# Optimization experiments

Measured on AMD Instinct MI355X. Metric: run time of the kernel, lower is better.

The kernel has to match this reference:

```python
import math
import jax, jax.numpy as jnp
import numpy as np

B, QC, KC, RES, SRC = 4, 512, 256, 64, 128
T = RES * RES


def setup_inputs():
    key = jax.random.key(0)
    ks = jax.random.split(key, 8)
    return {
        "key_feat": jax.random.normal(ks[0], (B, KC, SRC, SRC), jnp.float32),
        "query": jax.random.normal(ks[1], (B, QC, RES, RES), jnp.float32),
        "Weight_Mat": jax.random.uniform(ks[2], (B, T, T), dtype=jnp.float32),
        "key_proj_w": jax.random.normal(ks[3], (QC, KC), jnp.float32) * 0.02,
        "norm_w": jnp.ones((QC,), jnp.float32),
        "norm_b": jnp.zeros((QC,), jnp.float32),
        "qkv_w": jax.random.normal(ks[4], (3 * QC, 2 * QC), jnp.float32) * 0.02,
        "qkv_b": jax.random.normal(ks[5], (3 * QC,), jnp.float32) * 0.02,
        "proj_w": jax.random.normal(ks[6], (QC, QC), jnp.float32) * 0.02,
        "proj_b": jnp.zeros((QC,), jnp.float32),
    }


def group_norm(x, w, b, groups=32, eps=1e-5):
    # x: (b, C, L) -- GroupNorm over channel groups and spatial dim
    bs, C, L = x.shape
    xg = x.reshape(bs, groups, C // groups, L)
    mu = xg.mean(axis=(2, 3), keepdims=True)
    var = xg.var(axis=(2, 3), keepdims=True)
    xn = ((xg - mu) * jax.lax.rsqrt(var + eps)).reshape(bs, C, L)
    return xn * w[None, :, None] + b[None, :, None]


def reference(key_feat, query, Weight_Mat, key_proj_w, norm_w, norm_b, qkv_w, qkv_b, proj_w, proj_b):
    b, qc, H, W = query.shape
    f = key_feat.shape[2] // H  # exact integer downsample factor (2)
    # F.interpolate bilinear (align_corners=False) at exact 1/f rate == f x f average pooling
    kds = key_feat.reshape(b, key_feat.shape[1], H, f, W, f).mean(axis=(3, 5))
    # Weight_Mat interpolate has scale==1 in source (no-op), elided.
    k = jnp.einsum('oc,bchw->bohw', key_proj_w, kds).reshape(b, qc, H * W)
    q = query.reshape(b, qc, H * W)
    q = group_norm(q, norm_w, norm_b)
    k = group_norm(k, norm_w, norm_b)
    # qkv: 1x1 conv1d on concat(q, k) -> (b, 3*qc, T)
    qkv = jnp.einsum('oc,bct->bot', qkv_w, jnp.concatenate([q, k], axis=1)) + qkv_b[None, :, None]
    qq, kk, vv = jnp.split(qkv, 3, axis=1)  # each (b, qc, T); num_heads=1 so ch=qc
    scale = qc ** -0.25  # 1/sqrt(sqrt(ch))
    logits = Weight_Mat * jnp.einsum('bct,bcs->bts', qq * scale, kk * scale)
    attn = jax.nn.softmax(logits, axis=-1)
    a = jnp.einsum('bts,bcs->bct', attn, vv)
    h = jnp.einsum('oc,bct->bot', proj_w, a) + proj_b[None, :, None]
    # residual uses the NORMALIZED query, as in the source
    return (q + h).reshape(b, qc, H, W)
```

## Files before the change

kernel.cpp:

```cpp
#include <hip/hip_runtime.h>
#include <hip/hip_bf16.h>
#include <stdint.h>

#define NB 4
#define CQ 512
#define CK 256
#define TT 4096
#define SCALE_QK 0.21022410381342863f

using bf16x8 = __attribute__((ext_vector_type(8))) short;
using f32x4  = __attribute__((ext_vector_type(4))) float;
using u32x4  = __attribute__((ext_vector_type(4))) unsigned int;
typedef unsigned short u16;

__device__ __forceinline__ u16 f2bf(float f) {
    union { float f; unsigned u; } v; v.f = f;
    return (u16)((v.u + 0x7fffu + ((v.u >> 16) & 1u)) >> 16);
}
__device__ __forceinline__ float bf2f(u16 h) {
    union { float f; unsigned u; } v; v.u = ((unsigned)h) << 16;
    return v.f;
}
__device__ __forceinline__ bf16x8 pack8(f32x4 a, f32x4 b) {
    bf16x8 r;
    r[0] = (short)f2bf(a[0]); r[1] = (short)f2bf(a[1]);
    r[2] = (short)f2bf(a[2]); r[3] = (short)f2bf(a[3]);
    r[4] = (short)f2bf(b[0]); r[5] = (short)f2bf(b[1]);
    r[6] = (short)f2bf(b[2]); r[7] = (short)f2bf(b[3]);
    return r;
}
__device__ __forceinline__ void gload_lds16(const void* g, void* l) {
    __builtin_amdgcn_global_load_lds(
        (const __attribute__((address_space(1))) unsigned int*)g,
        (__attribute__((address_space(3))) unsigned int*)l, 16, 0, 0);
}

__global__ __launch_bounds__(256) void wconv_kernel(const float* __restrict__ src,
        u16* __restrict__ dst, int n, int scale_until) {
    int i = (blockIdx.x * 256 + threadIdx.x) * 8;
    if (i >= n) return;
    f32x4 a = *(const f32x4*)(src + i);
    f32x4 c = *(const f32x4*)(src + i + 4);
    if (i < scale_until) {
        a *= SCALE_QK;
        c *= SCALE_QK;
    }
    *(bf16x8*)(dst + i) = pack8(a, c);
}

__global__ __launch_bounds__(256) void pool_tr_kernel(const float* __restrict__ kf,
                                                      u16* __restrict__ kdsT) {
    int h = blockIdx.x, b = blockIdx.y;
    __shared__ u16 tile[64][264];
    for (int idx = threadIdx.x; idx < 64 * 256; idx += 256) {
        int w = idx & 63, c = idx >> 6;
        const float* base = kf + (((size_t)b * CK + c) * 128 + 2 * h) * 128 + 2 * w;
        float2 r0 = *(const float2*)base;
        float2 r1 = *(const float2*)(base + 128);
        tile[w][c] = f2bf(0.25f * (r0.x + r0.y + r1.x + r1.y));
    }
    __syncthreads();
    for (int idx = threadIdx.x; idx < 64 * 32; idx += 256) {
        int w = idx >> 5, cg = (idx & 31) << 3;
        *(u32x4*)(kdsT + ((size_t)b * TT + h * 64 + w) * CK + cg) = *(const u32x4*)&tile[w][cg];
    }
}

template <int ISBF>
__global__ __launch_bounds__(256) void gn_stats_kernel(const void* __restrict__ xv,
        const float* __restrict__ gw, const float* __restrict__ gb,
        float* __restrict__ sc, float* __restrict__ sh) {
    int g = blockIdx.x, b = blockIdx.y;
    size_t base = ((size_t)b * CQ + g * 16) * TT;
    float s = 0.f, q = 0.f;
    for (int i = threadIdx.x * 4; i < 16 * TT; i += 256 * 4) {
        float v0, v1, v2, v3;
        if constexpr (ISBF) {
            const u16* x = (const u16*)xv;
            uint2 u = *(const uint2*)(x + base + i);
            v0 = bf2f((u16)(u.x & 0xffff)); v1 = bf2f((u16)(u.x >> 16));
            v2 = bf2f((u16)(u.y & 0xffff)); v3 = bf2f((u16)(u.y >> 16));
        } else {
            const float* x = (const float*)xv;
            f32x4 v = *(const f32x4*)(x + base + i);
            v0 = v[0]; v1 = v[1]; v2 = v[2]; v3 = v[3];
        }
        s += v0 + v1 + v2 + v3;
        q += v0 * v0 + v1 * v1 + v2 * v2 + v3 * v3;
    }
#pragma unroll
    for (int d = 1; d < 64; d <<= 1) { s += __shfl_xor(s, d, 64); q += __shfl_xor(q, d, 64); }
    __shared__ float shs[4], shq[4];
    int wid = threadIdx.x >> 6;
    if ((threadIdx.x & 63) == 0) { shs[wid] = s; shq[wid] = q; }
    __syncthreads();
    if (threadIdx.x < 16) {
        float S = shs[0] + shs[1] + shs[2] + shs[3];
        float Q = shq[0] + shq[1] + shq[2] + shq[3];
        const float inv = 1.f / (16.f * TT);
        float mean = S * inv, var = Q * inv - mean * mean;
        float rstd = rsqrtf(var + 1e-5f);
        int c = g * 16 + threadIdx.x;
        float w = gw[c] * rstd;
        sc[b * CQ + c] = w;
        sh[b * CQ + c] = gb[c] - mean * w;
    }
}

template <int ISBF>
__global__ __launch_bounds__(256) void affine_tr_kernel(const void* __restrict__ xv,
        const float* __restrict__ sc, const float* __restrict__ sh, u16* __restrict__ out) {
    int t0 = blockIdx.x * 64, c0 = blockIdx.y * 64, b = blockIdx.z;
    __shared__ u16 tile[64][72];
    for (int idx = threadIdx.x; idx < 64 * 64; idx += 256) {
        int tl = idx & 63, cl = idx >> 6;
        int c = c0 + cl;
        float v;
        if constexpr (ISBF) v = bf2f(((const u16*)xv)[((size_t)b * CQ + c) * TT + t0 + tl]);
        else                v = ((const float*)xv)[((size_t)b * CQ + c) * TT + t0 + tl];
        tile[tl][cl] = f2bf(v * sc[b * CQ + c] + sh[b * CQ + c]);
    }
    __syncthreads();
    for (int idx = threadIdx.x; idx < 64 * 8; idx += 256) {
        int tl = idx >> 3, cg = (idx & 7) << 3;
        *(u32x4*)(out + ((size_t)b * TT + t0 + tl) * CQ + c0 + cg) = *(const u32x4*)&tile[tl][cg];
    }
}

template <int EPI, int CONCAT, int SWAP>
__global__ __launch_bounds__(256) void gemm_st_kernel(
        const u16* __restrict__ Wb, const u16* __restrict__ X1, const u16* __restrict__ X2,
        int Ktot, const float* __restrict__ bias,
        u16* __restrict__ outb, u16* __restrict__ outb2, float* __restrict__ outf,
        const float* __restrict__ query, const float* __restrict__ qsc,
        const float* __restrict__ qsh) {
    int b = blockIdx.z;
    int o0 = blockIdx.x * 128, t0 = blockIdx.y * 128;
    int wid = threadIdx.x >> 6, lane = threadIdx.x & 63;
    int lr = lane & 15, lg = lane >> 4;
    int osub = (wid >> 1) * 64, tsub = (wid & 1) * 64;

    __shared__ u16 Wl[2][128][64];
    __shared__ u16 Xl[2][128][64];

    const int Kx = CONCAT ? 512 : Ktot;
    int srow = lane >> 3;
    int sxw = ((lane & 7) ^ srow) << 4;
    int xr = (lr & 7) << 4;

    f32x4 acc[4][4];
#pragma unroll
    for (int i = 0; i < 4; i++)
#pragma unroll
        for (int j = 0; j < 4; j++) acc[i][j] = f32x4{0.f, 0.f, 0.f, 0.f};

    int nk = Ktot >> 6;

#define STAGE_TILE(KC, BUF)                                                          \
    do {                                                                             \
        int c0_ = (KC) << 6;                                                         \
        const u16* xs_;                                                              \
        if (CONCAT && c0_ >= 512) xs_ = X2 + ((size_t)b * TT) * 512 + (c0_ - 512);   \
        else if (CONCAT)          xs_ = X1 + ((size_t)b * TT) * 512 + c0_;           \
        else                      xs_ = X1 + ((size_t)b * TT) * (size_t)Ktot + c0_;  \
        const char* xb_ = (const char*)(xs_ + (size_t)(t0 + wid * 32) * Kx) + sxw;   \
        const char* wb_ = (const char*)(Wb + (size_t)(o0 + wid * 32) * Ktot + c0_) + sxw; \
        _Pragma("unroll")                                                            \
        for (int i_ = 0; i_ < 4; i_++) {                                             \
            gload_lds16(xb_ + (size_t)(i_ * 8 + srow) * (Kx * 2),                    \
                        &Xl[BUF][wid * 32 + i_ * 8][0]);                             \
            gload_lds16(wb_ + (size_t)(i_ * 8 + srow) * (Ktot * 2),                  \
                        &Wl[BUF][wid * 32 + i_ * 8][0]);                             \
        }                                                                            \
    } while (0)

    STAGE_TILE(0, 0);
    __syncthreads();
    int cur = 0;
    for (int kc = 0; kc < nk; kc++) {
        if (kc + 1 < nk) STAGE_TILE(kc + 1, cur ^ 1);
#pragma unroll
        for (int kk = 0; kk < 2; kk++) {
            int boff = (kk * 64 + lg * 16) ^ xr;
            bf16x8 am[4], bn[4];
#pragma unroll
            for (int mi = 0; mi < 4; mi++) {
                if (SWAP) am[mi] = *(const bf16x8*)((const char*)&Xl[cur][tsub + mi * 16 + lr][0] + boff);
                else      am[mi] = *(const bf16x8*)((const char*)&Wl[cur][osub + mi * 16 + lr][0] + boff);
            }
#pragma unroll
            for (int ni = 0; ni < 4; ni++) {
                if (SWAP) bn[ni] = *(const bf16x8*)((const char*)&Wl[cur][osub + ni * 16 + lr][0] + boff);
                else      bn[ni] = *(const bf16x8*)((const char*)&Xl[cur][tsub + ni * 16 + lr][0] + boff);
            }
#pragma unroll
            for (int mi = 0; mi < 4; mi++)
#pragma unroll
                for (int ni = 0; ni < 4; ni++)
                    acc[mi][ni] = __builtin_amdgcn_mfma_f32_16x16x32_bf16(am[mi], bn[ni], acc[mi][ni], 0, 0, 0);
        }
        __syncthreads();
        cur ^= 1;
    }
#undef STAGE_TILE

    if (SWAP) {
#pragma unroll
        for (int mi = 0; mi < 4; mi++)
#pragma unroll
            for (int ni = 0; ni < 4; ni++)
#pragma unroll
                for (int reg = 0; reg < 4; reg++) {
                    int t = t0 + tsub + mi * 16 + 4 * lg + reg;
                    int o = o0 + osub + ni * 16 + lr;
                    float v = acc[mi][ni][reg] + bias[o] * SCALE_QK;
                    if (o < 512) outb[((size_t)b * TT + t) * 512 + o] = f2bf(v);
                    else         outb2[((size_t)b * TT + t) * 512 + (o - 512)] = f2bf(v);
                }
    } else {
#pragma unroll
        for (int mi = 0; mi < 4; mi++)
#pragma unroll
            for (int reg = 0; reg < 4; reg++) {
                int o = o0 + osub + mi * 16 + 4 * lg + reg;
                float bv = (EPI >= 1) ? bias[o] : 0.f;
#pragma unroll
                for (int ni = 0; ni < 4; ni++) {
                    int t = t0 + tsub + ni * 16 + lr;
                    size_t oidx = ((size_t)b * CQ + o) * TT + t;
                    float v = acc[mi][ni][reg] + bv;
                    if (EPI == 2) {
                        outf[oidx] = v + query[oidx] * qsc[b * CQ + o] + qsh[b * CQ + o];
                    } else {
                        outb[oidx] = f2bf(v);
                    }
                }
            }
    }
}

__global__ __launch_bounds__(512, 2) void flash_kernel(
        const u16* __restrict__ qqT, const u16* __restrict__ kkT,
        const u16* __restrict__ vv, const float* __restrict__ WM,
        u16* __restrict__ aT) {
    int b = blockIdx.y;
    int T0 = blockIdx.x * 64;
    int wid = threadIdx.x >> 6, lane = threadIdx.x & 63;
    int lr = lane & 15, lg = lane >> 4;
    int tb = wid >> 1, sb = wid & 1;
    int tb2 = wid >> 2, sbq = wid & 3;

    __shared__ u16 K_lds[64][512];
    __shared__ u16 V_lds[512][64];
    __shared__ u16 p_lds[64][64];
    __shared__ float ex_max[64][2];
    __shared__ float ex_sum[64][2];
    __shared__ float m_lds[64];

    if (threadIdx.x < 64) m_lds[threadIdx.x] = 0.f;

    bf16x8 qf[16];
    {
        const u16* qrow = qqT + ((size_t)b * TT + T0 + 16 * tb + lr) * CQ + lg * 8;
#pragma unroll
        for (int kc = 0; kc < 16; kc++) qf[kc] = *(const bf16x8*)(qrow + kc * 32);
    }
    f32x4 acc[2][8];
#pragma unroll
    for (int i = 0; i < 2; i++)
#pragma unroll
        for (int j = 0; j < 8; j++) acc[i][j] = f32x4{0.f, 0.f, 0.f, 0.f};
    float m[2][4], l[2][4];
#pragma unroll
    for (int i = 0; i < 2; i++)
#pragma unroll
        for (int r = 0; r < 4; r++) { m[i][r] = 0.f; l[i][r] = 0.f; }

    const float* wmrow = WM + ((size_t)b * TT + T0 + 16 * tb + 4 * lg) * TT + 32 * sb + lr;
    const char* kbase = (const char*)(kkT + (size_t)b * TT * CQ);
    int myt = 16 * tb + 4 * lg;

    for (int s0 = 0; s0 < TT; s0 += 64) {
        __syncthreads();
#pragma unroll
        for (int i = 0; i < 8; i++) {
            int s = wid * 8 + i;
            gload_lds16(kbase + (size_t)(s0 + s) * 1024 + ((lane ^ (s & 7)) << 4),
                        &K_lds[s][0]);
        }
#pragma unroll
        for (int g2 = 0; g2 < 8; g2++) {
            int c0 = (wid * 8 + g2) * 8;
            int c = c0 + (lane >> 3);
            gload_lds16((const char*)(vv + ((size_t)b * CQ + c) * TT + s0) +
                            ((((lane & 7) ^ (c & 7))) << 4),
                        &V_lds[c0][0]);
        }
        float wmv[2][4];
#pragma unroll
        for (int fs = 0; fs < 2; fs++)
#pragma unroll
            for (int reg = 0; reg < 4; reg++)
                wmv[fs][reg] = wmrow[(size_t)reg * TT + s0 + fs * 16];
        float mq[4];
#pragma unroll
        for (int reg = 0; reg < 4; reg++) mq[reg] = m_lds[myt + reg];
        __syncthreads();

        f32x4 sacc[2];
        sacc[0] = f32x4{0.f, 0.f, 0.f, 0.f};
        sacc[1] = f32x4{0.f, 0.f, 0.f, 0.f};
#pragma unroll
        for (int kc = 0; kc < 16; kc++) {
#pragma unroll
            for (int fs = 0; fs < 2; fs++) {
                const char* kp = (const char*)&K_lds[32 * sb + fs * 16 + lr][0];
                bf16x8 kfr = *(const bf16x8*)(kp + ((((kc << 2) | lg) ^ (lr & 7)) << 4));
                sacc[fs] = __builtin_amdgcn_mfma_f32_16x16x32_bf16(qf[kc], kfr, sacc[fs], 0, 0, 0);
            }
        }
        float pmax[4], psum[4];
#pragma unroll
        for (int r = 0; r < 4; r++) { pmax[r] = -3e38f; psum[r] = 0.f; }
#pragma unroll
        for (int fs = 0; fs < 2; fs++)
#pragma unroll
            for (int reg = 0; reg < 4; reg++) {
                float v = sacc[fs][reg] * wmv[fs][reg];
                pmax[reg] = fmaxf(pmax[reg], v);
                float p = __expf(v - mq[reg]);
                psum[reg] += p;
                int t = myt + reg;
                int s = 32 * sb + fs * 16 + lr;
                *(u16*)((char*)p_lds + t * 128 + ((((s >> 3) ^ (t & 7))) << 4) + ((s & 7) << 1)) = f2bf(p);
            }
#pragma unroll
        for (int d = 1; d < 16; d <<= 1)
#pragma unroll
            for (int reg = 0; reg < 4; reg++) {
                pmax[reg] = fmaxf(pmax[reg], __shfl_xor(pmax[reg], d, 64));
                psum[reg] += __shfl_xor(psum[reg], d, 64);
            }
        if (lr == 0) {
#pragma unroll
            for (int reg = 0; reg < 4; reg++) {
                ex_max[myt + reg][sb] = pmax[reg];
                ex_sum[myt + reg][sb] = psum[reg];
            }
        }
        __syncthreads();

#pragma unroll
        for (int ks = 0; ks < 2; ks++) {
            bf16x8 pa[2];
#pragma unroll
            for (int mi = 0; mi < 2; mi++) {
                int prow = 32 * tb2 + mi * 16 + lr;
                pa[mi] = *(const bf16x8*)((const char*)p_lds + prow * 128 +
                                          ((((ks << 2) | lg) ^ (lr & 7)) << 4));
            }
#pragma unroll
            for (int nc = 0; nc < 8; nc++) {
                int vr = 128 * sbq + nc * 16 + lr;
                bf16x8 vf = *(const bf16x8*)((const char*)&V_lds[vr][0] +
                                             ((((ks << 2) | lg) ^ (lr & 7)) << 4));
#pragma unroll
                for (int mi = 0; mi < 2; mi++)
                    acc[mi][nc] = __builtin_amdgcn_mfma_f32_16x16x32_bf16(pa[mi], vf, acc[mi][nc], 0, 0, 0);
            }
        }
        bool needany = false;
        float fac[2][4];
#pragma unroll
        for (int mi = 0; mi < 2; mi++)
#pragma unroll
            for (int reg = 0; reg < 4; reg++) {
                int t = 32 * tb2 + mi * 16 + 4 * lg + reg;
                float pm = fmaxf(ex_max[t][0], ex_max[t][1]);
                l[mi][reg] += ex_sum[t][0] + ex_sum[t][1];
                if (pm > m[mi][reg] + 8.f) {
                    fac[mi][reg] = __expf(m[mi][reg] - pm);
                    m[mi][reg] = pm;
                    needany = true;
                } else {
                    fac[mi][reg] = 1.f;
                }
            }
        if (__any(needany)) {
#pragma unroll
            for (int mi = 0; mi < 2; mi++)
#pragma unroll
                for (int reg = 0; reg < 4; reg++) {
                    l[mi][reg] *= fac[mi][reg];
#pragma unroll
                    for (int nc = 0; nc < 8; nc++) acc[mi][nc][reg] *= fac[mi][reg];
                }
            if (lr == 0) {
#pragma unroll
                for (int mi = 0; mi < 2; mi++)
#pragma unroll
                    for (int reg = 0; reg < 4; reg++)
                        m_lds[32 * tb2 + mi * 16 + 4 * lg + reg] = m[mi][reg];
            }
        }
    }
    float inv[2][4];
#pragma unroll
    for (int mi = 0; mi < 2; mi++)
#pragma unroll
        for (int reg = 0; reg < 4; reg++) inv[mi][reg] = 1.f / l[mi][reg];
#pragma unroll
    for (int mi = 0; mi < 2; mi++)
#pragma unroll
        for (int nc = 0; nc < 8; nc++)
#pragma unroll
            for (int reg = 0; reg < 4; reg++) {
                int t = T0 + 32 * tb2 + mi * 16 + 4 * lg + reg;
                int c = 128 * sbq + nc * 16 + lr;
                aT[((size_t)b * TT + t) * CQ + c] = f2bf(acc[mi][nc][reg] * inv[mi][reg]);
            }
}

extern "C" void kernel_launch(void* const* d_in, const int* in_sizes, int n_in,
                              void* d_out, int out_size, void* d_ws, size_t ws_size,
                              hipStream_t stream) {
    const float* key_feat = (const float*)d_in[0];
    const float* query    = (const float*)d_in[1];
    const float* WM       = (const float*)d_in[2];
    const float* kpw      = (const float*)d_in[3];
    const float* norm_w   = (const float*)d_in[4];
    const float* norm_b   = (const float*)d_in[5];
    const float* qkv_w    = (const float*)d_in[6];
    const float* qkv_b    = (const float*)d_in[7];
    const float* proj_w   = (const float*)d_in[8];
    const float* proj_b   = (const float*)d_in[9];
    float* out = (float*)d_out;
    char* ws = (char*)d_ws;

    u16* kdsT = (u16*)(ws);
    u16* kraw = (u16*)(ws + 8388608);
    u16* qnT  = (u16*)(ws + 25165824);
    u16* knT  = (u16*)(ws + 41943040);
    u16* qqT  = (u16*)(ws + 58720256);
    u16* kkT  = (u16*)(ws + 75497472);
    u16* vvp  = (u16*)(ws + 92274688);
    u16* aT   = (u16*)(ws);
    u16* wqkv = (u16*)(ws + 16777216);
    u16* wproj= (u16*)(ws + 19922944);
    float* qsc = (float*)(ws + 109051904);
    float* qsh = qsc + NB * CQ;
    float* ksc = qsh + NB * CQ;
    float* ksh = ksc + NB * CQ;
    u16* wkp  = (u16*)(ws + 109084672);

    wconv_kernel<<<64, 256, 0, stream>>>(kpw, wkp, 512 * 256, 0);
    pool_tr_kernel<<<dim3(64, NB), 256, 0, stream>>>(key_feat, kdsT);
    gemm_st_kernel<0, 0, 0><<<dim3(4, 32, NB), 256, 0, stream>>>(
        wkp, kdsT, nullptr, CK, nullptr, kraw, nullptr, nullptr, nullptr, nullptr, nullptr);
    gn_stats_kernel<0><<<dim3(32, NB), 256, 0, stream>>>(query, norm_w, norm_b, qsc, qsh);
    gn_stats_kernel<1><<<dim3(32, NB), 256, 0, stream>>>(kraw, norm_w, norm_b, ksc, ksh);
    affine_tr_kernel<0><<<dim3(64, 8, NB), 256, 0, stream>>>(query, qsc, qsh, qnT);
    affine_tr_kernel<1><<<dim3(64, 8, NB), 256, 0, stream>>>(kraw, ksc, ksh, knT);
    wconv_kernel<<<768, 256, 0, stream>>>(qkv_w, wqkv, 1536 * 1024, 1024 * 1024);
    wconv_kernel<<<128, 256, 0, stream>>>(proj_w, wproj, 512 * 512, 0);
    gemm_st_kernel<1, 1, 1><<<dim3(8, 32, NB), 256, 0, stream>>>(
        wqkv, qnT, knT, 1024, qkv_b, qqT, kkT, nullptr, nullptr, nullptr, nullptr);
    gemm_st_kernel<1, 1, 0><<<dim3(4, 32, NB), 256, 0, stream>>>(
        wqkv + (size_t)1024 * 1024, qnT, knT, 1024, qkv_b + 1024, vvp, nullptr, nullptr,
        nullptr, nullptr, nullptr);
    flash_kernel<<<dim3(64, NB), 512, 0, stream>>>(qqT, kkT, vvp, WM, aT);
    gemm_st_kernel<2, 0, 0><<<dim3(4, 32, NB), 256, 0, stream>>>(
        wproj, aT, nullptr, CQ, proj_b, nullptr, nullptr, out, query, qsc, qsh);
}
```

Measured before the change: 551.8 us.

## Split flash attention over key dimension with combine kernel and smaller tiles

Splits the key/source dimension of the flash attention kernel into two chunks, giving twice as many workgroups (512 instead of 256). Each chunk writes normalized partial outputs plus its row max and sum, and a new combine kernel merges them. The key tile is halved to 32 to cut LDS use so more blocks fit per CU (launch bounds raised to 4). Syncthreads are replaced with explicit waitcnt and barrier asm plus sched barriers. This adds an extra kernel and a bf16 round trip of the partial outputs through memory, and it doubles the number of iterations with smaller MFMA work per barrier.

```diff
diff --git a/kernel.cpp b/kernel.cpp
--- a/kernel.cpp
+++ b/kernel.cpp
@@ -6,6 +6,8 @@
 #define CQ 512
 #define CK 256
 #define TT 4096
+#define NCH 2
+#define SCH (TT / NCH)
 #define SCALE_QK 0.21022410381342863f
 
 using bf16x8 = __attribute__((ext_vector_type(8))) short;
@@ -239,20 +241,20 @@
     }
 }
 
-__global__ __launch_bounds__(512, 2) void flash_kernel(
+__global__ __launch_bounds__(512, 4) void flash_kernel(
         const u16* __restrict__ qqT, const u16* __restrict__ kkT,
         const u16* __restrict__ vv, const float* __restrict__ WM,
-        u16* __restrict__ aT) {
-    int b = blockIdx.y;
+        u16* __restrict__ pacc, float* __restrict__ pm, float* __restrict__ pl) {
+    int b = blockIdx.z, ch = blockIdx.y;
     int T0 = blockIdx.x * 64;
     int wid = threadIdx.x >> 6, lane = threadIdx.x & 63;
     int lr = lane & 15, lg = lane >> 4;
     int tb = wid >> 1, sb = wid & 1;
     int tb2 = wid >> 2, sbq = wid & 3;
 
-    __shared__ u16 K_lds[64][512];
-    __shared__ u16 V_lds[512][64];
-    __shared__ u16 p_lds[64][64];
+    __shared__ u16 K_lds[32][512];
+    __shared__ u16 V_lds[512][32];
+    __shared__ u16 p_lds[64][32];
     __shared__ float ex_max[64][2];
     __shared__ float ex_sum[64][2];
     __shared__ float m_lds[64];
@@ -276,64 +278,63 @@
 #pragma unroll
         for (int r = 0; r < 4; r++) { m[i][r] = 0.f; l[i][r] = 0.f; }
 
-    const float* wmrow = WM + ((size_t)b * TT + T0 + 16 * tb + 4 * lg) * TT + 32 * sb + lr;
+    const float* wmrow = WM + ((size_t)b * TT + T0 + 16 * tb + 4 * lg) * TT + 16 * sb + lr;
     const char* kbase = (const char*)(kkT + (size_t)b * TT * CQ);
+    const char* vbase = (const char*)(vv + (size_t)b * CQ * TT);
     int myt = 16 * tb + 4 * lg;
-
-    for (int s0 = 0; s0 < TT; s0 += 64) {
-        __syncthreads();
-#pragma unroll
-        for (int i = 0; i < 8; i++) {
-            int s = wid * 8 + i;
+    int sbeg = ch * SCH;
+
+#pragma unroll 1
+    for (int it = 0; it < SCH / 32; it++) {
+        int s0 = sbeg + it * 32;
+        asm volatile("s_waitcnt lgkmcnt(0)\ns_barrier" ::: "memory");
+#pragma unroll
+        for (int i = 0; i < 4; i++) {
+            int s = 4 * wid + i;
             gload_lds16(kbase + (size_t)(s0 + s) * 1024 + ((lane ^ (s & 7)) << 4),
                         &K_lds[s][0]);
         }
-#pragma unroll
-        for (int g2 = 0; g2 < 8; g2++) {
-            int c0 = (wid * 8 + g2) * 8;
-            int c = c0 + (lane >> 3);
-            gload_lds16((const char*)(vv + ((size_t)b * CQ + c) * TT + s0) +
-                            ((((lane & 7) ^ (c & 7))) << 4),
+        __builtin_amdgcn_sched_barrier(0);
+#pragma unroll
+        for (int g = 0; g < 4; g++) {
+            int c0 = 64 * wid + 16 * g;
+            int c = c0 + (lane >> 2);
+            gload_lds16(vbase + (size_t)c * (TT * 2) + (size_t)s0 * 2 +
+                            ((((lane & 3) ^ ((c >> 1) & 3))) << 4),
                         &V_lds[c0][0]);
         }
-        float wmv[2][4];
-#pragma unroll
-        for (int fs = 0; fs < 2; fs++)
-#pragma unroll
-            for (int reg = 0; reg < 4; reg++)
-                wmv[fs][reg] = wmrow[(size_t)reg * TT + s0 + fs * 16];
+        __builtin_amdgcn_sched_barrier(0);
+        float wmv[4];
+#pragma unroll
+        for (int r = 0; r < 4; r++) wmv[r] = wmrow[(size_t)r * TT + s0];
         float mq[4];
 #pragma unroll
-        for (int reg = 0; reg < 4; reg++) mq[reg] = m_lds[myt + reg];
-        __syncthreads();
-
-        f32x4 sacc[2];
-        sacc[0] = f32x4{0.f, 0.f, 0.f, 0.f};
-        sacc[1] = f32x4{0.f, 0.f, 0.f, 0.f};
-#pragma unroll
-        for (int kc = 0; kc < 16; kc++) {
-#pragma unroll
-            for (int fs = 0; fs < 2; fs++) {
-                const char* kp = (const char*)&K_lds[32 * sb + fs * 16 + lr][0];
-                bf16x8 kfr = *(const bf16x8*)(kp + ((((kc << 2) | lg) ^ (lr & 7)) << 4));
-                sacc[fs] = __builtin_amdgcn_mfma_f32_16x16x32_bf16(qf[kc], kfr, sacc[fs], 0, 0, 0);
+        for (int r = 0; r < 4; r++) mq[r] = m_lds[myt + r];
+        __builtin_amdgcn_sched_barrier(0);
+        asm volatile("s_waitcnt vmcnt(8)\ns_barrier" ::: "memory");
+
+        f32x4 sacc = f32x4{0.f, 0.f, 0.f, 0.f};
+        {
+            int srow = 16 * sb + lr;
+            const char* kp = (const char*)&K_lds[srow][0];
+            int sw = srow & 7;
+#pragma unroll
+            for (int kc = 0; kc < 16; kc++) {
+                bf16x8 kfr = *(const bf16x8*)(kp + ((((kc << 2) | lg) ^ sw) << 4));
+                sacc = __builtin_amdgcn_mfma_f32_16x16x32_bf16(qf[kc], kfr, sacc, 0, 0, 0);
             }
         }
         float pmax[4], psum[4];
 #pragma unroll
-        for (int r = 0; r < 4; r++) { pmax[r] = -3e38f; psum[r] = 0.f; }
-#pragma unroll
-        for (int fs = 0; fs < 2; fs++)
-#pragma unroll
-            for (int reg = 0; reg < 4; reg++) {
-                float v = sacc[fs][reg] * wmv[fs][reg];
-                pmax[reg] = fmaxf(pmax[reg], v);
-                float p = __expf(v - mq[reg]);
-                psum[reg] += p;
-                int t = myt + reg;
-                int s = 32 * sb + fs * 16 + lr;
-                *(u16*)((char*)p_lds + t * 128 + ((((s >> 3) ^ (t & 7))) << 4) + ((s & 7) << 1)) = f2bf(p);
-            }
+        for (int reg = 0; reg < 4; reg++) {
+            float v = sacc[reg] * wmv[reg];
+            pmax[reg] = v;
+            float p = __expf(v - mq[reg]);
+            psum[reg] = p;
+            int t = myt + reg;
+            int s = 16 * sb + lr;
+            *(u16*)((char*)p_lds + t * 64 + ((((s >> 3) ^ ((t >> 1) & 3))) << 4) + ((s & 7) << 1)) = f2bf(p);
+        }
 #pragma unroll
         for (int d = 1; d < 16; d <<= 1)
 #pragma unroll
@@ -348,22 +349,21 @@
                 ex_sum[myt + reg][sb] = psum[reg];
             }
         }
-        __syncthreads();
-
-#pragma unroll
-        for (int ks = 0; ks < 2; ks++) {
+        asm volatile("s_waitcnt vmcnt(0) lgkmcnt(0)\ns_barrier" ::: "memory");
+
+        {
             bf16x8 pa[2];
 #pragma unroll
             for (int mi = 0; mi < 2; mi++) {
                 int prow = 32 * tb2 + mi * 16 + lr;
-                pa[mi] = *(const bf16x8*)((const char*)p_lds + prow * 128 +
-                                          ((((ks << 2) | lg) ^ (lr & 7)) << 4));
+                pa[mi] = *(const bf16x8*)((const char*)p_lds + prow * 64 +
+                                          ((lg ^ ((prow >> 1) & 3)) << 4));
             }
 #pragma unroll
             for (int nc = 0; nc < 8; nc++) {
                 int vr = 128 * sbq + nc * 16 + lr;
-                bf16x8 vf = *(const bf16x8*)((const char*)&V_lds[vr][0] +
-                                             ((((ks << 2) | lg) ^ (lr & 7)) << 4));
+                bf16x8 vf = *(const bf16x8*)((const char*)V_lds + vr * 64 +
+                                             ((lg ^ ((vr >> 1) & 3)) << 4));
 #pragma unroll
                 for (int mi = 0; mi < 2; mi++)
                     acc[mi][nc] = __builtin_amdgcn_mfma_f32_16x16x32_bf16(pa[mi], vf, acc[mi][nc], 0, 0, 0);
@@ -376,11 +376,11 @@
 #pragma unroll
             for (int reg = 0; reg < 4; reg++) {
                 int t = 32 * tb2 + mi * 16 + 4 * lg + reg;
-                float pm = fmaxf(ex_max[t][0], ex_max[t][1]);
+                float pmx = fmaxf(ex_max[t][0], ex_max[t][1]);
                 l[mi][reg] += ex_sum[t][0] + ex_sum[t][1];
-                if (pm > m[mi][reg] + 8.f) {
-                    fac[mi][reg] = __expf(m[mi][reg] - pm);
-                    m[mi][reg] = pm;
+                if (pmx > m[mi][reg] + 8.f) {
+                    fac[mi][reg] = __expf(m[mi][reg] - pmx);
+                    m[mi][reg] = pmx;
                     needany = true;
                 } else {
                     fac[mi][reg] = 1.f;
@@ -409,6 +409,7 @@
     for (int mi = 0; mi < 2; mi++)
 #pragma unroll
         for (int reg = 0; reg < 4; reg++) inv[mi][reg] = 1.f / l[mi][reg];
+    size_t row = (size_t)(ch * NB + b) * TT;
 #pragma unroll
     for (int mi = 0; mi < 2; mi++)
 #pragma unroll
@@ -417,8 +418,41 @@
             for (int reg = 0; reg < 4; reg++) {
                 int t = T0 + 32 * tb2 + mi * 16 + 4 * lg + reg;
                 int c = 128 * sbq + nc * 16 + lr;
-                aT[((size_t)b * TT + t) * CQ + c] = f2bf(acc[mi][nc][reg] * inv[mi][reg]);
-            }
+                pacc[(row + t) * CQ + c] = f2bf(acc[mi][nc][reg] * inv[mi][reg]);
+            }
+    if (sbq == 0 && lr == 0) {
+#pragma unroll
+        for (int mi = 0; mi < 2; mi++)
+#pragma unroll
+            for (int reg = 0; reg < 4; reg++) {
+                int t = T0 + 32 * tb2 + mi * 16 + 4 * lg + reg;
+                pm[row + t] = m[mi][reg];
+                pl[row + t] = l[mi][reg];
+            }
+    }
+}
+
+__global__ __launch_bounds__(256) void combine_kernel(
+        const u16* __restrict__ pacc, const float* __restrict__ pm,
+        const float* __restrict__ pl, u16* __restrict__ aT) {
+    int b = blockIdx.y;
+    int t = blockIdx.x * 4 + (threadIdx.x >> 6);
+    int cg = (threadIdx.x & 63) * 8;
+    size_t r0 = (size_t)(0 * NB + b) * TT + t;
+    size_t r1 = (size_t)(1 * NB + b) * TT + t;
+    float m0 = pm[r0], m1 = pm[r1];
+    float l0 = pl[r0], l1 = pl[r1];
+    float M = fmaxf(m0, m1);
+    float w0 = l0 * __expf(m0 - M), w1 = l1 * __expf(m1 - M);
+    float inv = 1.f / (w0 + w1);
+    w0 *= inv; w1 *= inv;
+    bf16x8 a0 = *(const bf16x8*)(pacc + r0 * CQ + cg);
+    bf16x8 a1 = *(const bf16x8*)(pacc + r1 * CQ + cg);
+    bf16x8 o;
+#pragma unroll
+    for (int j = 0; j < 8; j++)
+        o[j] = (short)f2bf(bf2f((u16)a0[j]) * w0 + bf2f((u16)a1[j]) * w1);
+    *(bf16x8*)(aT + ((size_t)b * TT + t) * CQ + cg) = o;
 }
 
 extern "C" void kernel_launch(void* const* d_in, const int* in_sizes, int n_in,
@@ -441,12 +475,15 @@
     u16* kraw = (u16*)(ws + 8388608);
     u16* qnT  = (u16*)(ws + 25165824);
     u16* knT  = (u16*)(ws + 41943040);
+    u16* pacc = (u16*)(ws + 25165824);
     u16* qqT  = (u16*)(ws + 58720256);
     u16* kkT  = (u16*)(ws + 75497472);
     u16* vvp  = (u16*)(ws + 92274688);
     u16* aT   = (u16*)(ws);
     u16* wqkv = (u16*)(ws + 16777216);
     u16* wproj= (u16*)(ws + 19922944);
+    float* pm = (float*)(ws + 20447232);
+    float* pl = (float*)(ws + 20578304);
     float* qsc = (float*)(ws + 109051904);
     float* qsh = qsc + NB * CQ;
     float* ksc = qsh + NB * CQ;
@@ -468,7 +505,8 @@
     gemm_st_kernel<1, 1, 0><<<dim3(4, 32, NB), 256, 0, stream>>>(
         wqkv + (size_t)1024 * 1024, qnT, knT, 1024, qkv_b + 1024, vvp, nullptr, nullptr,
         nullptr, nullptr, nullptr);
-    flash_kernel<<<dim3(64, NB), 512, 0, stream>>>(qqT, kkT, vvp, WM, aT);
+    flash_kernel<<<dim3(64, NCH, NB), 512, 0, stream>>>(qqT, kkT, vvp, WM, pacc, pm, pl);
+    combine_kernel<<<dim3(TT / 4, NB), 256, 0, stream>>>(pacc, pm, pl, aT);
     gemm_st_kernel<2, 0, 0><<<dim3(4, 32, NB), 256, 0, stream>>>(
         wproj, aT, nullptr, CQ, proj_b, nullptr, nullptr, out, query, qsc, qsh);
 }
```

Result: slower. 1.257 ms (+127.8%).
